# Performance work log

Hardware: AMD Instinct MI355X
Metric: run time of the kernel (lower is better)

## Reference

```python
import jax, jax.numpy as jnp
import numpy as np

B, S, H, V = 2, 2048, 2048, 128000

def setup_inputs() -> dict:
    key = jax.random.key(0)
    kx, ky, kw = jax.random.split(key, 3)
    x = jax.random.normal(kx, (B, S, H), dtype=jnp.float32)
    y = jax.random.randint(ky, (B, S), 0, V, dtype=jnp.int64)
    # nn.Linear default init: U(-1/sqrt(H), 1/sqrt(H))
    bound = 1.0 / np.sqrt(H)
    W = jax.random.uniform(kw, (V, H), dtype=jnp.float32, minval=-bound, maxval=bound)
    return {"x": x, "y": y, "W": W}

def reference(x, y, W):
    # logits: [B*S, V]
    xf = x.reshape(-1, x.shape[-1])            # [N, H]
    logits = jnp.einsum('nh,vh->nv', xf, W)    # [N, V]
    logp = jax.nn.log_softmax(logits, axis=-1)
    yf = y.reshape(-1)
    nll = -jnp.take_along_axis(logp, yf[:, None], axis=-1)[:, 0]
    return jnp.mean(nll)
```

## Files before the change

### kernel.cpp

```cpp
#include <hip/hip_runtime.h>

typedef unsigned short u16;
typedef unsigned char u8;
typedef unsigned int u32;
typedef long long i64;
typedef __attribute__((ext_vector_type(4))) int i32x4;
typedef __attribute__((ext_vector_type(8))) short short8;
typedef __attribute__((ext_vector_type(4))) float f32x4;

constexpr int HD = 2048;
constexpr int NR = 4096;
constexpr int VO = 128000;

constexpr int NMB9 = NR / 128;
constexpr int NVB8 = VO / 256;
constexpr int NT8  = HD / 64;
constexpr float XSCALE = 24.0f;
constexpr float WSCALE = 5700.0f;
constexpr float UNSCALE = 1.0f / (XSCALE * WSCALE);

constexpr size_t OFF_X8  = 0;
constexpr size_t OFF_W8  = 8388608;
constexpr size_t OFF_PMX = OFF_W8 + 262144000;
constexpr size_t OFF_PSM = OFF_PMX + 8192000;
constexpr size_t OFF_LSE = OFF_PSM + 8192000;
constexpr size_t OFF_TL  = OFF_LSE + 16384;
constexpr size_t NEED_NEW = OFF_TL + 16384;

constexpr int NVBF = VO / 128;
constexpr int NMBF = NR / 128;
constexpr size_t FB_XB   = 0;
constexpr size_t FB_PMAX = 16777216;
constexpr size_t FB_PSUM = FB_PMAX + 16384000;
constexpr size_t FB_LSE  = FB_PSUM + 16384000;
constexpr size_t FB_TL   = FB_LSE + (size_t)NR * 4;

__device__ __forceinline__ u32 swz16(u32 a) { return a ^ (((a >> 7) & 3u) << 4); }

__device__ __forceinline__ u8 q8(float f) {
  int t = __float2int_rn(f);
  t = t > 127 ? 127 : (t < -127 ? -127 : t);
  return (u8)(char)t;
}

__global__ __launch_bounds__(256) void cvt_x8_kernel(const float* __restrict__ x,
                                                     u8* __restrict__ x8) {
  const long i = (long)blockIdx.x * 256 + threadIdx.x;
  const float4* X4 = reinterpret_cast<const float4*>(x) + i * 4;
  union { u8 b[16]; uint4 v; } p;
#pragma unroll
  for (int j = 0; j < 4; ++j) {
    float4 a = X4[j];
    p.b[j * 4 + 0] = q8(a.x * XSCALE);
    p.b[j * 4 + 1] = q8(a.y * XSCALE);
    p.b[j * 4 + 2] = q8(a.z * XSCALE);
    p.b[j * 4 + 3] = q8(a.w * XSCALE);
  }
  reinterpret_cast<uint4*>(x8)[i] = p.v;
}

__global__ __launch_bounds__(256) void cvt_w8_kernel(const float* __restrict__ W,
                                                     u8* __restrict__ w8) {
  const long total = (long)VO * HD / 16;
  long i = (long)blockIdx.x * 256 + threadIdx.x;
  const long stride = (long)gridDim.x * 256;
  for (; i < total; i += stride) {
    const float4* W4 = reinterpret_cast<const float4*>(W) + i * 4;
    union { u8 b[16]; uint4 v; } p;
#pragma unroll
    for (int j = 0; j < 4; ++j) {
      float4 a = W4[j];
      p.b[j * 4 + 0] = q8(a.x * WSCALE);
      p.b[j * 4 + 1] = q8(a.y * WSCALE);
      p.b[j * 4 + 2] = q8(a.z * WSCALE);
      p.b[j * 4 + 3] = q8(a.w * WSCALE);
    }
    reinterpret_cast<uint4*>(w8)[i] = p.v;
  }
}

__global__ __launch_bounds__(512, 4) void gemm8(
    const u8* __restrict__ x8, const u8* __restrict__ w8,
    float* __restrict__ pmax, float* __restrict__ psum) {
  __shared__ uint4 smem4[4608];
  __shared__ float smax[128][4];
  __shared__ float ssum[128][4];
  char* Sm = reinterpret_cast<char*>(smem4);

  const int tid = threadIdx.x;
  const int w = tid >> 6, l = tid & 63;
  const int wr = w >> 2, wc = w & 3;
  const int q = l >> 4, r15 = l & 15;

  const int bid = blockIdx.x;
  const int s = (bid & 7) * 2000 + (bid >> 3);
  const int mb = s & 31;
  const int vb = s >> 5;
  const int rowbase = mb * 128, vbase = vb * 256;

  const u8* aS; const u8* bS0; const u8* bS1;
  {
    u32 lin = (u32)tid * 16u;
    u32 r = lin >> 6, qq = ((lin >> 4) & 3u) ^ ((r >> 2) & 3u);
    aS  = x8 + (size_t)(rowbase + (int)r) * HD + qq * 16u;
    bS0 = w8 + (size_t)(vbase  + (int)r) * HD + qq * 16u;
    bS1 = bS0 + (size_t)128 * HD;
  }
  const u32 dA  = (u32)(w * 1024);
  const u32 dB0 = 8192u + (u32)(w * 1024);
  const u32 dB1 = 16384u + (u32)(w * 1024);

  auto stg = [&](const u8* src, u32 dstOff) {
    __builtin_amdgcn_global_load_lds(
        (const __attribute__((address_space(1))) u32*)src,
        (__attribute__((address_space(3))) u32*)(Sm + dstOff), 16, 0, 0);
  };
#define STAGE(T, OFF) do {                      \
    stg(aS  + (size_t)(T) * 64, (OFF) + dA);    \
    stg(bS0 + (size_t)(T) * 64, (OFF) + dB0);   \
    stg(bS1 + (size_t)(T) * 64, (OFF) + dB1);   \
  } while (0)

  const u32 slot = ((u32)q ^ ((u32)(r15 >> 2))) << 4;
  const u32 aBase = ((u32)(wr * 64 + r15) << 6) + slot;
  const u32 bBase = 8192u + ((u32)(wc * 64 + r15) << 6) + slot;

  union U4 { uint4 v; i32x4 s; };
  U4 aF[4], bF[4];
  i32x4 acc[4][4];
#pragma unroll
  for (int m = 0; m < 4; ++m)
#pragma unroll
    for (int n = 0; n < 4; ++n) acc[m][n] = (i32x4)(0);

#define SCH() __builtin_amdgcn_sched_barrier(0)
#define RDA(JJ) aF[JJ].v = *reinterpret_cast<const uint4*>(Sm + rdOff + aBase + (JJ) * 1024)
#define RDB(NN) bF[NN].v = *reinterpret_cast<const uint4*>(Sm + rdOff + bBase + (NN) * 1024)
#define MM1(JJ, NN) acc[JJ][NN] = __builtin_amdgcn_mfma_i32_16x16x64_i8( \
    aF[JJ].s, bF[NN].s, acc[JJ][NN], 0, 0, 0)

  STAGE(0, 0u);
  STAGE(1, 24576u);
  u32 rdOff = 0u;
  u32 stOff = 49152u;

  for (int t = 0; t < NT8; ++t) {
    if (t + 1 < NT8) asm volatile("s_waitcnt vmcnt(3)" ::: "memory");
    else             asm volatile("s_waitcnt vmcnt(0)" ::: "memory");
    __builtin_amdgcn_s_barrier();
    SCH();
    RDB(0); RDA(0);
    SCH();
    __builtin_amdgcn_s_setprio(1);
    MM1(0, 0); SCH(); RDB(1); SCH();
    MM1(0, 1); SCH(); RDB(2); SCH();
    MM1(0, 2); SCH(); RDB(3); SCH();
    MM1(0, 3); SCH(); RDA(1); SCH();
    MM1(1, 0); SCH(); RDA(2); SCH();
    MM1(1, 1); MM1(1, 2); MM1(1, 3); SCH(); RDA(3); SCH();
    MM1(2, 0); MM1(2, 1);
    SCH();
    if (t + 2 < NT8) { STAGE(t + 2, stOff); }
    SCH();
    MM1(2, 2); MM1(2, 3);
    MM1(3, 0); MM1(3, 1); MM1(3, 2); MM1(3, 3);
    __builtin_amdgcn_s_setprio(0);
    SCH();
    rdOff = (rdOff == 49152u) ? 0u : rdOff + 24576u;
    stOff = (stOff == 49152u) ? 0u : stOff + 24576u;
  }
#undef MM1
#undef RDA
#undef RDB
#undef SCH
#undef STAGE

#pragma unroll
  for (int jj = 0; jj < 4; ++jj) {
#pragma unroll
    for (int j = 0; j < 4; ++j) {
      float v0 = (float)acc[jj][0][j] * UNSCALE, v1 = (float)acc[jj][1][j] * UNSCALE;
      float v2 = (float)acc[jj][2][j] * UNSCALE, v3 = (float)acc[jj][3][j] * UNSCALE;
      float mx = fmaxf(fmaxf(v0, v1), fmaxf(v2, v3));
#pragma unroll
      for (int d = 1; d < 16; d <<= 1) mx = fmaxf(mx, __shfl_xor(mx, d));
      float se = __expf(v0 - mx) + __expf(v1 - mx) + __expf(v2 - mx) + __expf(v3 - mx);
#pragma unroll
      for (int d = 1; d < 16; d <<= 1) se += __shfl_xor(se, d);
      if (r15 == 0) {
        int r = wr * 64 + jj * 16 + q * 4 + j;
        smax[r][wc] = mx;
        ssum[r][wc] = se;
      }
    }
  }
  __syncthreads();
  if (tid < 128) {
    float m0 = smax[tid][0], m1 = smax[tid][1], m2 = smax[tid][2], m3 = smax[tid][3];
    float M = fmaxf(fmaxf(m0, m1), fmaxf(m2, m3));
    float S = ssum[tid][0] * __expf(m0 - M) + ssum[tid][1] * __expf(m1 - M) +
              ssum[tid][2] * __expf(m2 - M) + ssum[tid][3] * __expf(m3 - M);
    size_t o = (size_t)vb * NR + (size_t)(rowbase + tid);
    pmax[o] = M;
    psum[o] = S;
  }
}

__global__ __launch_bounds__(256) void cvt_x_kernel(const float* __restrict__ x,
                                                    u16* __restrict__ xb) {
  int i = blockIdx.x * 256 + threadIdx.x;
  float4 v = reinterpret_cast<const float4*>(x)[i];
  union { __bf16 b[4]; unsigned long long ll; } p;
  p.b[0] = (__bf16)v.x; p.b[1] = (__bf16)v.y;
  p.b[2] = (__bf16)v.z; p.b[3] = (__bf16)v.w;
  reinterpret_cast<unsigned long long*>(xb)[i] = p.ll;
}

__global__ __launch_bounds__(256) void gemm_partials_fb(
    const u16* __restrict__ xb, const float* __restrict__ W,
    float* __restrict__ pmax, float* __restrict__ psum) {
  __shared__ uint4 smem[1024];
  __shared__ float smax[128][2];
  __shared__ float ssum[128][2];
  char* Ab = reinterpret_cast<char*>(smem);
  char* Bb = Ab + 8192;

  const int tid = threadIdx.x;
  const int w = tid >> 6;
  const int l = tid & 63;
  const int wr = w >> 1, wc = w & 1;

  const int bid = blockIdx.x;
  const int s = (bid & 7) * (NMBF * NVBF / 8) + (bid >> 3);
  const int mb = s & (NMBF - 1);
  const int vb = s >> 5;
  const int rowbase = mb * 128;
  const int vbase = vb * 128;

  const u16* aSrc[2];
  unsigned aBase[2];
#pragma unroll
  for (int i = 0; i < 2; ++i) {
    unsigned lin = (unsigned)w * 2048u + (unsigned)i * 1024u + (unsigned)l * 16u;
    unsigned sb = swz16(lin);
    unsigned r = sb >> 6;
    unsigned c = (sb >> 1) & 31u;
    aSrc[i] = xb + (size_t)(rowbase + (int)r) * HD + c;
    aBase[i] = (unsigned)w * 2048u + (unsigned)i * 1024u;
  }
  const float* bSrc[2];
  unsigned bLin[2];
#pragma unroll
  for (int i = 0; i < 2; ++i) {
    unsigned lin = (unsigned)i * 4096u + (unsigned)tid * 16u;
    unsigned sb = swz16(lin);
    unsigned n = sb >> 6;
    unsigned k = (sb >> 1) & 31u;
    bSrc[i] = W + (size_t)(vbase + (int)n) * HD + k;
    bLin[i] = lin;
  }
  const unsigned q = (unsigned)(l >> 4);
  unsigned aOff[4], bOff[4];
#pragma unroll
  for (int m = 0; m < 4; ++m) {
    unsigned R = (unsigned)(wr * 64 + m * 16 + (l & 15));
    aOff[m] = swz16(R * 64u + q * 16u);
    R = (unsigned)(wc * 64 + m * 16 + (l & 15));
    bOff[m] = swz16(R * 64u + q * 16u);
  }
  f32x4 acc[4][4];
#pragma unroll
  for (int m = 0; m < 4; ++m)
#pragma unroll
    for (int n = 0; n < 4; ++n) acc[m][n] = (f32x4)(0.0f);

  for (int kt = 0; kt < HD; kt += 32) {
    float4 g0 = *reinterpret_cast<const float4*>(bSrc[0]);
    float4 g1 = *reinterpret_cast<const float4*>(bSrc[0] + 4);
    float4 g2 = *reinterpret_cast<const float4*>(bSrc[1]);
    float4 g3 = *reinterpret_cast<const float4*>(bSrc[1] + 4);
#pragma unroll
    for (int i = 0; i < 2; ++i) {
      __builtin_amdgcn_global_load_lds(
          (const __attribute__((address_space(1))) u32*)aSrc[i],
          (__attribute__((address_space(3))) u32*)(Ab + aBase[i]), 16, 0, 0);
    }
    union { __bf16 b[8]; uint4 v; } p0, p1;
    p0.b[0] = (__bf16)g0.x; p0.b[1] = (__bf16)g0.y; p0.b[2] = (__bf16)g0.z; p0.b[3] = (__bf16)g0.w;
    p0.b[4] = (__bf16)g1.x; p0.b[5] = (__bf16)g1.y; p0.b[6] = (__bf16)g1.z; p0.b[7] = (__bf16)g1.w;
    p1.b[0] = (__bf16)g2.x; p1.b[1] = (__bf16)g2.y; p1.b[2] = (__bf16)g2.z; p1.b[3] = (__bf16)g2.w;
    p1.b[4] = (__bf16)g3.x; p1.b[5] = (__bf16)g3.y; p1.b[6] = (__bf16)g3.z; p1.b[7] = (__bf16)g3.w;
    *reinterpret_cast<uint4*>(Bb + bLin[0]) = p0.v;
    *reinterpret_cast<uint4*>(Bb + bLin[1]) = p1.v;
    __syncthreads();

    short8 af[4], bfr[4];
#pragma unroll
    for (int m = 0; m < 4; ++m) af[m] = *reinterpret_cast<const short8*>(Ab + aOff[m]);
#pragma unroll
    for (int n = 0; n < 4; ++n) bfr[n] = *reinterpret_cast<const short8*>(Bb + bOff[n]);
#pragma unroll
    for (int m = 0; m < 4; ++m)
#pragma unroll
      for (int n = 0; n < 4; ++n)
        acc[m][n] = __builtin_amdgcn_mfma_f32_16x16x32_bf16(af[m], bfr[n], acc[m][n], 0, 0, 0);
    __syncthreads();

    aSrc[0] += 32; aSrc[1] += 32;
    bSrc[0] += 32; bSrc[1] += 32;
  }
#pragma unroll
  for (int m = 0; m < 4; ++m) {
#pragma unroll
    for (int j = 0; j < 4; ++j) {
      float v0 = acc[m][0][j], v1 = acc[m][1][j], v2 = acc[m][2][j], v3 = acc[m][3][j];
      float mx = fmaxf(fmaxf(v0, v1), fmaxf(v2, v3));
#pragma unroll
      for (int d = 1; d < 16; d <<= 1) mx = fmaxf(mx, __shfl_xor(mx, d));
      float se = __expf(v0 - mx) + __expf(v1 - mx) + __expf(v2 - mx) + __expf(v3 - mx);
#pragma unroll
      for (int d = 1; d < 16; d <<= 1) se += __shfl_xor(se, d);
      if ((l & 15) == 0) {
        int rloc = wr * 64 + m * 16 + (int)q * 4 + j;
        smax[rloc][wc] = mx;
        ssum[rloc][wc] = se;
      }
    }
  }
  __syncthreads();
  if (tid < 128) {
    float m0 = smax[tid][0], m1 = smax[tid][1];
    float M = fmaxf(m0, m1);
    float S = ssum[tid][0] * __expf(m0 - M) + ssum[tid][1] * __expf(m1 - M);
    size_t o = (size_t)vb * NR + (size_t)(rowbase + tid);
    pmax[o] = M;
    psum[o] = S;
  }
}

__global__ __launch_bounds__(256) void row_lse_kernel(const float* __restrict__ pmax,
                                                      const float* __restrict__ psum,
                                                      float* __restrict__ lse, int nvb) {
  __shared__ float lm[4][64];
  __shared__ float ls[4][64];
  const int rb = blockIdx.x * 64;
  const int rl = threadIdx.x & 63;
  const int g = threadIdx.x >> 6;
  const int r = rb + rl;
  float M = -3.0e38f, S = 0.0f;
  for (int v = g; v < nvb; v += 4) {
    float m = pmax[(size_t)v * NR + r];
    float s = psum[(size_t)v * NR + r];
    float nM = fmaxf(M, m);
    S = S * __expf(M - nM) + s * __expf(m - nM);
    M = nM;
  }
  lm[g][rl] = M; ls[g][rl] = S;
  __syncthreads();
  if (threadIdx.x < 64) {
    float M0 = lm[0][rl], S0 = ls[0][rl];
#pragma unroll
    for (int g2 = 1; g2 < 4; ++g2) {
      float m = lm[g2][rl], s2 = ls[g2][rl];
      float nM = fmaxf(M0, m);
      S0 = S0 * __expf(M0 - nM) + s2 * __expf(m - nM);
      M0 = nM;
    }
    lse[r] = M0 + logf(S0);
  }
}

__global__ __launch_bounds__(256) void tlogit_kernel(const float* __restrict__ x,
                                                     const int* __restrict__ y,
                                                     const float* __restrict__ W,
                                                     float* __restrict__ tl) {
  const int row = blockIdx.x * 4 + (threadIdx.x >> 6);
  const int l = threadIdx.x & 63;
  const int t = y[row];
  const float4* xr = reinterpret_cast<const float4*>(x + (size_t)row * HD);
  const float4* wr = reinterpret_cast<const float4*>(W + (size_t)t * HD);
  float s = 0.0f;
#pragma unroll
  for (int i = 0; i < HD / 4 / 64; ++i) {
    float4 a = xr[l + i * 64];
    float4 b = wr[l + i * 64];
    s += a.x * b.x + a.y * b.y + a.z * b.z + a.w * b.w;
  }
#pragma unroll
  for (int d = 1; d < 64; d <<= 1) s += __shfl_xor(s, d);
  if (l == 0) tl[row] = s;
}

__global__ __launch_bounds__(256) void finalize_kernel(const float* __restrict__ lse,
                                                       const float* __restrict__ tl,
                                                       float* __restrict__ out) {
  __shared__ float red[256];
  float s = 0.0f;
  for (int i = threadIdx.x; i < NR; i += 256) s += lse[i] - tl[i];
  red[threadIdx.x] = s;
  __syncthreads();
  for (int d = 128; d > 0; d >>= 1) {
    if ((int)threadIdx.x < d) red[threadIdx.x] += red[threadIdx.x + d];
    __syncthreads();
  }
  if (threadIdx.x == 0) out[0] = red[0] * (1.0f / NR);
}

extern "C" void kernel_launch(void* const* d_in, const int* in_sizes, int n_in,
                              void* d_out, int out_size, void* d_ws, size_t ws_size,
                              hipStream_t stream) {
  const float* x = (const float*)d_in[0];
  const int* y = (const int*)d_in[1];
  const float* W = (const float*)d_in[2];
  float* out = (float*)d_out;
  char* ws = (char*)d_ws;

  if (ws_size >= NEED_NEW) {
    u8* x8      = (u8*)(ws + OFF_X8);
    u8* w8      = (u8*)(ws + OFF_W8);
    float* pmax = (float*)(ws + OFF_PMX);
    float* psum = (float*)(ws + OFF_PSM);
    float* lse  = (float*)(ws + OFF_LSE);
    float* tl   = (float*)(ws + OFF_TL);
    cvt_x8_kernel<<<NR * HD / 16 / 256, 256, 0, stream>>>(x, x8);
    cvt_w8_kernel<<<4096, 256, 0, stream>>>(W, w8);
    gemm8<<<NMB9 * NVB8, 512, 0, stream>>>(x8, w8, pmax, psum);
    row_lse_kernel<<<NR / 64, 256, 0, stream>>>(pmax, psum, lse, NVB8);
    tlogit_kernel<<<NR / 4, 256, 0, stream>>>(x, y, W, tl);
    finalize_kernel<<<1, 256, 0, stream>>>(lse, tl, out);
  } else {
    u16* xb     = (u16*)(ws + FB_XB);
    float* pmax = (float*)(ws + FB_PMAX);
    float* psum = (float*)(ws + FB_PSUM);
    float* lse  = (float*)(ws + FB_LSE);
    float* tl   = (float*)(ws + FB_TL);
    cvt_x_kernel<<<NR * HD / 4 / 256, 256, 0, stream>>>(x, xb);
    gemm_partials_fb<<<NMBF * NVBF, 256, 0, stream>>>(xb, W, pmax, psum);
    row_lse_kernel<<<NR / 64, 256, 0, stream>>>(pmax, psum, lse, NVBF);
    tlogit_kernel<<<NR / 4, 256, 0, stream>>>(x, y, W, tl);
    finalize_kernel<<<1, 256, 0, stream>>>(lse, tl, out);
  }
}
```

Measured before the change: 1.530 ms.

## Prefetch next tile's B fragments from LDS during current tile's MFMAs

```diff
diff --git a/kernel.cpp b/kernel.cpp
--- a/kernel.cpp
+++ b/kernel.cpp
@@ -135,43 +135,64 @@
 
 #define SCH() __builtin_amdgcn_sched_barrier(0)
 #define RDA(JJ) aF[JJ].v = *reinterpret_cast<const uint4*>(Sm + rdOff + aBase + (JJ) * 1024)
-#define RDB(NN) bF[NN].v = *reinterpret_cast<const uint4*>(Sm + rdOff + bBase + (NN) * 1024)
+#define RDBP(NN) bF[NN].v = *reinterpret_cast<const uint4*>(Sm + pfOff + bBase + (NN) * 1024)
 #define MM1(JJ, NN) acc[JJ][NN] = __builtin_amdgcn_mfma_i32_16x16x64_i8( \
     aF[JJ].s, bF[NN].s, acc[JJ][NN], 0, 0, 0)
 
   STAGE(0, 0u);
   STAGE(1, 24576u);
+  asm volatile("s_waitcnt vmcnt(0)" ::: "memory");
+  __builtin_amdgcn_s_barrier();
+  SCH();
+  {
+    const u32 pfOff = 0u;
+    RDBP(0); RDBP(1); RDBP(2); RDBP(3);
+  }
   u32 rdOff = 0u;
+  u32 pfOff = 24576u;
   u32 stOff = 49152u;
 
   for (int t = 0; t < NT8; ++t) {
-    if (t + 1 < NT8) asm volatile("s_waitcnt vmcnt(3)" ::: "memory");
-    else             asm volatile("s_waitcnt vmcnt(0)" ::: "memory");
     __builtin_amdgcn_s_barrier();
     SCH();
-    RDB(0); RDA(0);
+    RDA(0); RDA(1); RDA(2); RDA(3);
     SCH();
     __builtin_amdgcn_s_setprio(1);
-    MM1(0, 0); SCH(); RDB(1); SCH();
-    MM1(0, 1); SCH(); RDB(2); SCH();
-    MM1(0, 2); SCH(); RDB(3); SCH();
-    MM1(0, 3); SCH(); RDA(1); SCH();
-    MM1(1, 0); SCH(); RDA(2); SCH();
-    MM1(1, 1); MM1(1, 2); MM1(1, 3); SCH(); RDA(3); SCH();
-    MM1(2, 0); MM1(2, 1);
-    SCH();
+    MM1(0, 0); MM1(1, 0); MM1(2, 0); MM1(3, 0);
+    __builtin_amdgcn_s_setprio(0);
+    SCH();
+    if (t + 1 < NT8) {
+      asm volatile("s_waitcnt vmcnt(0)" ::: "memory");
+      __builtin_amdgcn_s_barrier();
+      SCH();
+      RDBP(0);
+      SCH();
+    }
+    __builtin_amdgcn_s_setprio(1);
+    MM1(0, 1); MM1(1, 1); MM1(2, 1); MM1(3, 1);
+    __builtin_amdgcn_s_setprio(0);
+    SCH();
+    if (t + 1 < NT8) { RDBP(1); SCH(); }
+    __builtin_amdgcn_s_setprio(1);
+    MM1(0, 2); MM1(1, 2); MM1(2, 2); MM1(3, 2);
+    __builtin_amdgcn_s_setprio(0);
+    SCH();
+    if (t + 1 < NT8) { RDBP(2); SCH(); }
+    __builtin_amdgcn_s_setprio(1);
+    MM1(0, 3); MM1(1, 3); MM1(2, 3); MM1(3, 3);
+    __builtin_amdgcn_s_setprio(0);
+    SCH();
+    if (t + 1 < NT8) { RDBP(3); SCH(); }
     if (t + 2 < NT8) { STAGE(t + 2, stOff); }
     SCH();
-    MM1(2, 2); MM1(2, 3);
-    MM1(3, 0); MM1(3, 1); MM1(3, 2); MM1(3, 3);
-    __builtin_amdgcn_s_setprio(0);
-    SCH();
-    rdOff = (rdOff == 49152u) ? 0u : rdOff + 24576u;
-    stOff = (stOff == 49152u) ? 0u : stOff + 24576u;
+    const u32 old = rdOff;
+    rdOff = pfOff;
+    pfOff = stOff;
+    stOff = old;
   }
 #undef MM1
+#undef RDBP
 #undef RDA
-#undef RDB
 #undef SCH
 #undef STAGE
 
```

After: 1.688 ms. 1.1x slower.
